# Kernel optimization log

Measured on AMD Instinct MI355X. Metric: run time of the kernel, lower is better.

## Reference

```python
import jax, jax.numpy as jnp
import numpy as np

B, T, C, H = 2048, 128, 256, 64

def setup_inputs() -> dict:
    key = jax.random.key(0)
    kx, kk, kq, kv = jax.random.split(key, 4)
    s = 1.0 / np.sqrt(C)  # nn.Linear default init scale (approx)
    return {
        "x": jax.random.normal(kx, (B, T, C), dtype=jnp.float32),
        "Wk": jax.random.uniform(kk, (C, H), jnp.float32, -s, s),
        "Wq": jax.random.uniform(kq, (C, H), jnp.float32, -s, s),
        "Wv": jax.random.uniform(kv, (C, H), jnp.float32, -s, s),
    }

def reference(x, Wk, Wq, Wv):
    # x: [B,T,C]; projections to [B,T,H]
    k = jnp.einsum('btc,ch->bth', x, Wk)
    q = jnp.einsum('btc,ch->bth', x, Wq)
    v = jnp.einsum('btc,ch->bth', x, Wv)
    # NOTE: original scales by C**-0.5 (input dim), not head_size**-0.5
    scale = jnp.asarray(C, x.dtype) ** -0.5
    wei = jnp.einsum('bth,bsh->bts', q, k) * scale  # [B,T,T]
    causal = jnp.tril(jnp.ones((T, T), dtype=bool))
    wei = jnp.where(causal, wei, -jnp.inf)
    wei = jax.nn.softmax(wei, axis=-1)
    # dropout is identity in eval mode (deterministic reference)
    return jnp.einsum('bts,bsh->bth', wei, v)
```

## Files before the change

kernel.cpp:

```cpp
#include <hip/hip_runtime.h>

typedef __bf16 bf16;
typedef __bf16 bf16x4 __attribute__((ext_vector_type(4)));
typedef __bf16 bf16x8 __attribute__((ext_vector_type(8)));
typedef float  f32x4  __attribute__((ext_vector_type(4)));

#define B_ 2048
#define T_ 128
#define C_ 256
#define H_ 64

#define SMEM_BYTES 54272

__global__ void wt_kernel(const float* __restrict__ Wk, const float* __restrict__ Wq,
                          const float* __restrict__ Wv, bf16* __restrict__ Wt) {
    int o = blockIdx.x * 256 + threadIdx.x;
    int slot = o >> 14;
    int r    = o & 16383;
    int cc   = r >> 6;
    int h    = r & 63;
    const float* src = (slot == 0) ? Wq : (slot == 1 ? Wk : Wv);
    Wt[slot * 16384 + h * 256 + cc] = (bf16)src[r];
}

__global__ void __launch_bounds__(256, 3)
attn_kernel(const float* __restrict__ xg, const bf16* __restrict__ Wt,
            float* __restrict__ outg) {
    __shared__ __align__(16) char smem_raw[SMEM_BYTES];
    bf16* xb0 = (bf16*)smem_raw;
    bf16* xb1 = (bf16*)(smem_raw + 18432);
    bf16* Qs  = (bf16*)smem_raw;
    bf16* Ks  = (bf16*)(smem_raw + 18432);
    bf16* Vt  = (bf16*)(smem_raw + 36864);
    bf16* Ps  = (bf16*)smem_raw;
    float* Of = (float*)smem_raw;

    const int tid  = threadIdx.x;
    const int b    = blockIdx.x;
    const int w    = tid >> 6;
    const int lane = tid & 63;
    const int quad = lane >> 4;
    const int n16  = lane & 15;

    const f32x4 zero4 = {0.f, 0.f, 0.f, 0.f};

    f32x4 acc[2][12];
    #pragma unroll
    for (int mt = 0; mt < 2; mt++)
        #pragma unroll
        for (int nt = 0; nt < 12; nt++) acc[mt][nt] = zero4;

    const float*  xb  = xg + (size_t)b * (T_ * C_);
    const ushort* WtU = (const ushort*)Wt;

    float4 xr[8];
    #pragma unroll
    for (int i = 0; i < 8; i++) {
        int f = tid + 256 * i;
        int t = f >> 4, c4 = (f & 15) * 4;
        xr[i] = *(const float4*)(xb + t * C_ + c4);
    }
    #pragma unroll
    for (int i = 0; i < 8; i++) {
        int f = tid + 256 * i;
        int t = f >> 4, c4 = (f & 15) * 4;
        bf16x4 bv = {(bf16)xr[i].x, (bf16)xr[i].y, (bf16)xr[i].z, (bf16)xr[i].w};
        *(bf16x4*)(xb0 + t * 72 + c4) = bv;
    }

    for (int c = 0; c < 4; c++) {
        if (c < 3) {
            #pragma unroll
            for (int i = 0; i < 8; i++) {
                int f = tid + 256 * i;
                int t = f >> 4, c4 = (f & 15) * 4;
                xr[i] = *(const float4*)(xb + t * C_ + (c + 1) * 64 + c4);
            }
        }
        __syncthreads();
        const bf16* xs = (c & 1) ? xb1 : xb0;
        bf16x8 a[2][2];
        #pragma unroll
        for (int mt = 0; mt < 2; mt++)
            #pragma unroll
            for (int ks = 0; ks < 2; ks++)
                a[mt][ks] = *(const bf16x8*)(xs + (16 * (2 * w + mt) + n16) * 72 + 32 * ks + 8 * quad);
        #pragma unroll
        for (int nt = 0; nt < 12; nt++) {
            const ushort* wp = WtU + (nt >> 2) * 16384 + (16 * (nt & 3) + n16) * 256 + c * 64 + 8 * quad;
            bf16x8 b0 = *(const bf16x8*)(wp);
            bf16x8 b1 = *(const bf16x8*)(wp + 32);
            #pragma unroll
            for (int mt = 0; mt < 2; mt++) {
                acc[mt][nt] = __builtin_amdgcn_mfma_f32_16x16x32_bf16(a[mt][0], b0, acc[mt][nt], 0, 0, 0);
                acc[mt][nt] = __builtin_amdgcn_mfma_f32_16x16x32_bf16(a[mt][1], b1, acc[mt][nt], 0, 0, 0);
            }
        }
        if (c < 3) {
            bf16* dstb = (c & 1) ? xb0 : xb1;
            #pragma unroll
            for (int i = 0; i < 8; i++) {
                int f = tid + 256 * i;
                int t = f >> 4, c4 = (f & 15) * 4;
                bf16x4 bv = {(bf16)xr[i].x, (bf16)xr[i].y, (bf16)xr[i].z, (bf16)xr[i].w};
                *(bf16x4*)(dstb + t * 72 + c4) = bv;
            }
        }
    }
    __syncthreads();

    #pragma unroll
    for (int mt = 0; mt < 2; mt++) {
        int tbase = 16 * (2 * w + mt) + 4 * quad;
        #pragma unroll
        for (int nt = 0; nt < 8; nt++) {
            bf16* dst = (nt < 4) ? Qs : Ks;
            int h = 16 * (nt & 3) + n16;
            #pragma unroll
            for (int r = 0; r < 4; r++)
                dst[(tbase + r) * 72 + h] = (bf16)acc[mt][nt][r];
        }
        #pragma unroll
        for (int nt = 8; nt < 12; nt++) {
            int h = 16 * (nt - 8) + n16;
            bf16x4 pv = {(bf16)acc[mt][nt][0], (bf16)acc[mt][nt][1],
                         (bf16)acc[mt][nt][2], (bf16)acc[mt][nt][3]};
            *(bf16x4*)(Vt + h * 136 + tbase) = pv;
        }
    }
    __syncthreads();

    f32x4 sacc[2][8];
    int mts[2] = {w, 7 - w};
    #pragma unroll
    for (int half = 0; half < 2; half++) {
        int mt = mts[half];
        int sT = ((mt >> 1) + 1) * 2;
        bf16x8 qa[2];
        #pragma unroll
        for (int ks = 0; ks < 2; ks++)
            qa[ks] = *(const bf16x8*)(Qs + (16 * mt + n16) * 72 + 32 * ks + 8 * quad);
        #pragma unroll
        for (int nt = 0; nt < 8; nt++) {
            sacc[half][nt] = zero4;
            if (nt < sT) {
                bf16x8 kb0 = *(const bf16x8*)(Ks + (16 * nt + n16) * 72 + 8 * quad);
                bf16x8 kb1 = *(const bf16x8*)(Ks + (16 * nt + n16) * 72 + 32 + 8 * quad);
                sacc[half][nt] = __builtin_amdgcn_mfma_f32_16x16x32_bf16(qa[0], kb0, sacc[half][nt], 0, 0, 0);
                sacc[half][nt] = __builtin_amdgcn_mfma_f32_16x16x32_bf16(qa[1], kb1, sacc[half][nt], 0, 0, 0);
            }
        }
        #pragma unroll
        for (int r = 0; r < 4; r++) {
            int t = 16 * mt + 4 * quad + r;
            float mx = -3.0e38f;
            #pragma unroll
            for (int nt = 0; nt < 8; nt++) {
                if (nt < sT) {
                    float v = sacc[half][nt][r] * 0.0625f;
                    v = (16 * nt + n16 <= t) ? v : -3.0e38f;
                    sacc[half][nt][r] = v;
                    mx = fmaxf(mx, v);
                }
            }
            mx = fmaxf(mx, __shfl_xor(mx, 1));
            mx = fmaxf(mx, __shfl_xor(mx, 2));
            mx = fmaxf(mx, __shfl_xor(mx, 4));
            mx = fmaxf(mx, __shfl_xor(mx, 8));
            float sum = 0.f;
            #pragma unroll
            for (int nt = 0; nt < 8; nt++) {
                if (nt < sT) {
                    float p = __builtin_amdgcn_exp2f((sacc[half][nt][r] - mx) * 1.4426950408889634f);
                    sacc[half][nt][r] = p;
                    sum += p;
                }
            }
            sum += __shfl_xor(sum, 1);
            sum += __shfl_xor(sum, 2);
            sum += __shfl_xor(sum, 4);
            sum += __shfl_xor(sum, 8);
            float rinv = 1.0f / sum;
            #pragma unroll
            for (int nt = 0; nt < 8; nt++)
                if (nt < sT) sacc[half][nt][r] *= rinv;
        }
    }
    __syncthreads();

    #pragma unroll
    for (int half = 0; half < 2; half++) {
        int mt = mts[half];
        int sT = ((mt >> 1) + 1) * 2;
        #pragma unroll
        for (int nt = 0; nt < 8; nt++) {
            if (nt < sT) {
                #pragma unroll
                for (int r = 0; r < 4; r++)
                    Ps[(16 * mt + 4 * quad + r) * 136 + 16 * nt + n16] = (bf16)sacc[half][nt][r];
            }
        }
    }
    __syncthreads();

    f32x4 oacc[2][4];
    #pragma unroll
    for (int half = 0; half < 2; half++) {
        int mt  = mts[half];
        int kst = (mt >> 1) + 1;
        #pragma unroll
        for (int nt = 0; nt < 4; nt++) oacc[half][nt] = zero4;
        #pragma unroll
        for (int ks = 0; ks < 4; ks++) {
            if (ks < kst) {
                bf16x8 pa = *(const bf16x8*)(Ps + (16 * mt + n16) * 136 + 32 * ks + 8 * quad);
                #pragma unroll
                for (int nt = 0; nt < 4; nt++) {
                    bf16x8 vb = *(const bf16x8*)(Vt + (16 * nt + n16) * 136 + 32 * ks + 8 * quad);
                    oacc[half][nt] = __builtin_amdgcn_mfma_f32_16x16x32_bf16(pa, vb, oacc[half][nt], 0, 0, 0);
                }
            }
        }
    }
    __syncthreads();

    #pragma unroll
    for (int half = 0; half < 2; half++) {
        int mt = mts[half];
        #pragma unroll
        for (int nt = 0; nt < 4; nt++)
            #pragma unroll
            for (int r = 0; r < 4; r++)
                Of[(16 * mt + 4 * quad + r) * 68 + 16 * nt + n16] = oacc[half][nt][r];
    }
    __syncthreads();
    #pragma unroll
    for (int i = 0; i < 8; i++) {
        int f = tid + 256 * i;
        int t = f >> 4, h4 = (f & 15) * 4;
        float4 v = *(const float4*)(Of + t * 68 + h4);
        *(float4*)(outg + ((size_t)b * T_ + t) * H_ + h4) = v;
    }
}

extern "C" void kernel_launch(void* const* d_in, const int* in_sizes, int n_in,
                              void* d_out, int out_size, void* d_ws, size_t ws_size,
                              hipStream_t stream) {
    const float* x  = (const float*)d_in[0];
    const float* Wk = (const float*)d_in[1];
    const float* Wq = (const float*)d_in[2];
    const float* Wv = (const float*)d_in[3];
    bf16* Wt = (bf16*)d_ws;
    wt_kernel<<<192, 256, 0, stream>>>(Wk, Wq, Wv, Wt);
    attn_kernel<<<B_, 256, 0, stream>>>(x, Wt, (float*)d_out);
}
```

Before: 541.6 us.

## Stage full x tile in LDS upfront instead of double-buffered 64-channel chunks

Loads all of x (128x256) into LDS as bf16 with a register double-buffered global prefetch, then runs the projection GEMM as one fully unrolled 8-step K loop without the per-chunk barriers. This removes the three inner syncthreads and the overlap of conversion with MFMA work, in exchange for a larger LDS footprint (about 66 KB), which lowers the occupancy target from 3 to 2 blocks per CU. Global loads become fully coalesced 1 KB row reads.

```diff
diff --git a/kernel.cpp b/kernel.cpp
--- a/kernel.cpp
+++ b/kernel.cpp
@@ -10,7 +10,7 @@
 #define C_ 256
 #define H_ 64
 
-#define SMEM_BYTES 54272
+#define SMEM_BYTES 67584
 
 __global__ void wt_kernel(const float* __restrict__ Wk, const float* __restrict__ Wq,
                           const float* __restrict__ Wv, bf16* __restrict__ Wt) {
@@ -23,12 +23,11 @@
     Wt[slot * 16384 + h * 256 + cc] = (bf16)src[r];
 }
 
-__global__ void __launch_bounds__(256, 3)
+__global__ void __launch_bounds__(256, 2)
 attn_kernel(const float* __restrict__ xg, const bf16* __restrict__ Wt,
             float* __restrict__ outg) {
     __shared__ __align__(16) char smem_raw[SMEM_BYTES];
-    bf16* xb0 = (bf16*)smem_raw;
-    bf16* xb1 = (bf16*)(smem_raw + 18432);
+    bf16* xs  = (bf16*)smem_raw;
     bf16* Qs  = (bf16*)smem_raw;
     bf16* Ks  = (bf16*)(smem_raw + 18432);
     bf16* Vt  = (bf16*)(smem_raw + 36864);
@@ -43,68 +42,56 @@
     const int n16  = lane & 15;
 
     const f32x4 zero4 = {0.f, 0.f, 0.f, 0.f};
-
-    f32x4 acc[2][12];
-    #pragma unroll
-    for (int mt = 0; mt < 2; mt++)
-        #pragma unroll
-        for (int nt = 0; nt < 12; nt++) acc[mt][nt] = zero4;
-
     const float*  xb  = xg + (size_t)b * (T_ * C_);
     const ushort* WtU = (const ushort*)Wt;
 
-    float4 xr[8];
-    #pragma unroll
-    for (int i = 0; i < 8; i++) {
-        int f = tid + 256 * i;
-        int t = f >> 4, c4 = (f & 15) * 4;
-        xr[i] = *(const float4*)(xb + t * C_ + c4);
-    }
-    #pragma unroll
-    for (int i = 0; i < 8; i++) {
-        int f = tid + 256 * i;
-        int t = f >> 4, c4 = (f & 15) * 4;
-        bf16x4 bv = {(bf16)xr[i].x, (bf16)xr[i].y, (bf16)xr[i].z, (bf16)xr[i].w};
-        *(bf16x4*)(xb0 + t * 72 + c4) = bv;
-    }
-
-    for (int c = 0; c < 4; c++) {
-        if (c < 3) {
+    {
+        float4 xa[8], xb4[8];
+        #pragma unroll
+        for (int i = 0; i < 8; i++) {
+            int f = i * 256 + tid;
+            xa[i] = *(const float4*)(xb + (f >> 6) * C_ + (f & 63) * 4);
+        }
+        #pragma unroll
+        for (int g = 0; g < 4; g++) {
+            float4* cur = (g & 1) ? xb4 : xa;
+            float4* nxt = (g & 1) ? xa : xb4;
+            if (g < 3) {
+                #pragma unroll
+                for (int i = 0; i < 8; i++) {
+                    int f = (g + 1) * 2048 + i * 256 + tid;
+                    nxt[i] = *(const float4*)(xb + (f >> 6) * C_ + (f & 63) * 4);
+                }
+            }
             #pragma unroll
             for (int i = 0; i < 8; i++) {
-                int f = tid + 256 * i;
-                int t = f >> 4, c4 = (f & 15) * 4;
-                xr[i] = *(const float4*)(xb + t * C_ + (c + 1) * 64 + c4);
-            }
-        }
-        __syncthreads();
-        const bf16* xs = (c & 1) ? xb1 : xb0;
-        bf16x8 a[2][2];
+                int f = g * 2048 + i * 256 + tid;
+                int t = f >> 6, c4 = (f & 63) * 4;
+                bf16x4 bv = {(bf16)cur[i].x, (bf16)cur[i].y, (bf16)cur[i].z, (bf16)cur[i].w};
+                *(bf16x4*)(xs + t * 264 + c4) = bv;
+            }
+        }
+    }
+    __syncthreads();
+
+    f32x4 acc[2][12];
+    #pragma unroll
+    for (int mt = 0; mt < 2; mt++)
+        #pragma unroll
+        for (int nt = 0; nt < 12; nt++) acc[mt][nt] = zero4;
+
+    #pragma unroll
+    for (int ks = 0; ks < 8; ks++) {
+        bf16x8 a[2];
         #pragma unroll
         for (int mt = 0; mt < 2; mt++)
-            #pragma unroll
-            for (int ks = 0; ks < 2; ks++)
-                a[mt][ks] = *(const bf16x8*)(xs + (16 * (2 * w + mt) + n16) * 72 + 32 * ks + 8 * quad);
+            a[mt] = *(const bf16x8*)(xs + (16 * (2 * w + mt) + n16) * 264 + ks * 32 + 8 * quad);
         #pragma unroll
         for (int nt = 0; nt < 12; nt++) {
-            const ushort* wp = WtU + (nt >> 2) * 16384 + (16 * (nt & 3) + n16) * 256 + c * 64 + 8 * quad;
-            bf16x8 b0 = *(const bf16x8*)(wp);
-            bf16x8 b1 = *(const bf16x8*)(wp + 32);
-            #pragma unroll
-            for (int mt = 0; mt < 2; mt++) {
-                acc[mt][nt] = __builtin_amdgcn_mfma_f32_16x16x32_bf16(a[mt][0], b0, acc[mt][nt], 0, 0, 0);
-                acc[mt][nt] = __builtin_amdgcn_mfma_f32_16x16x32_bf16(a[mt][1], b1, acc[mt][nt], 0, 0, 0);
-            }
-        }
-        if (c < 3) {
-            bf16* dstb = (c & 1) ? xb0 : xb1;
-            #pragma unroll
-            for (int i = 0; i < 8; i++) {
-                int f = tid + 256 * i;
-                int t = f >> 4, c4 = (f & 15) * 4;
-                bf16x4 bv = {(bf16)xr[i].x, (bf16)xr[i].y, (bf16)xr[i].z, (bf16)xr[i].w};
-                *(bf16x4*)(dstb + t * 72 + c4) = bv;
-            }
+            const ushort* wp = WtU + (nt >> 2) * 16384 + (16 * (nt & 3) + n16) * 256 + ks * 32 + 8 * quad;
+            bf16x8 bfr = *(const bf16x8*)wp;
+            acc[0][nt] = __builtin_amdgcn_mfma_f32_16x16x32_bf16(a[0], bfr, acc[0][nt], 0, 0, 0);
+            acc[1][nt] = __builtin_amdgcn_mfma_f32_16x16x32_bf16(a[1], bfr, acc[1][nt], 0, 0, 0);
         }
     }
     __syncthreads();
```

Measured after the change: 472.9 us. 12.7% less time.
